# Optimization experiments

Hardware: AMD Instinct MI355X
Metric: run time of the kernel (lower is better)

Reference implementation:

```python
import jax, jax.numpy as jnp
import numpy as np

WS = 7        # window size
H = 32; W = 32  # input resolution
NH = 12       # num heads
HD = 32       # head dim (key_dim; attn_ratio=1 so d == key_dim)
DIM = 384
EPS = 1e-5


def _make_bias_idxs():
    # replicate itertools.product offset-insertion order: idx = |dy|*WS + |dx|
    coords = np.array(list(np.ndindex(WS, WS)))              # [N,2]
    off = np.abs(coords[:, None, :] - coords[None, :, :])    # [N,N,2]
    return jnp.asarray(off[..., 0] * WS + off[..., 1], dtype=jnp.int64)


def setup_inputs() -> dict:
    key = jax.random.key(0)
    ks = jax.random.split(key, 8)
    B = 32
    s = 0.02
    return {
        "x": jax.random.normal(ks[0], (B, H * W, DIM), jnp.float32),
        "ln1_w": jnp.ones((DIM,), jnp.float32),
        "ln1_b": jnp.zeros((DIM,), jnp.float32),
        "qkv_w": jax.random.normal(ks[1], (DIM, 3 * DIM), jnp.float32) * s,
        "qkv_b": jnp.zeros((3 * DIM,), jnp.float32),
        "proj_w": jax.random.normal(ks[2], (DIM, DIM), jnp.float32) * s,
        "proj_b": jnp.zeros((DIM,), jnp.float32),
        "attn_bias": jax.random.normal(ks[3], (NH, WS * WS), jnp.float32) * s,
        "bias_idxs": _make_bias_idxs(),
        "conv_w": jax.random.normal(ks[4], (DIM, 1, 3, 3), jnp.float32) * s,
        "bn_g": jnp.ones((DIM,), jnp.float32),
        "bn_b": jnp.zeros((DIM,), jnp.float32),
        "bn_m": jax.random.normal(ks[5], (DIM,), jnp.float32) * s,
        "bn_v": jax.random.uniform(ks[6], (DIM,), jnp.float32, 0.5, 1.5),
        "ln2_w": jnp.ones((DIM,), jnp.float32),
        "ln2_b": jnp.zeros((DIM,), jnp.float32),
        "fc1_w": jax.random.normal(ks[7], (DIM, 4 * DIM), jnp.float32) * s,
        "fc1_b": jnp.zeros((4 * DIM,), jnp.float32),
        "fc2_w": jax.random.normal(jax.random.fold_in(key, 9), (4 * DIM, DIM), jnp.float32) * s,
        "fc2_b": jnp.zeros((DIM,), jnp.float32),
    }


def _layernorm(x, w, b):
    mu = x.mean(-1, keepdims=True)
    var = x.var(-1, keepdims=True)
    return (x - mu) * jax.lax.rsqrt(var + EPS) * w + b


def reference(x, ln1_w, ln1_b, qkv_w, qkv_b, proj_w, proj_b, attn_bias,
              bias_idxs, conv_w, bn_g, bn_b, bn_m, bn_v,
              ln2_w, ln2_b, fc1_w, fc1_b, fc2_w, fc2_b):
    B, L, C = x.shape
    res = x
    # --- window partition (with bottom/right padding) ---
    pad_b = (WS - H % WS) % WS
    pad_r = (WS - W % WS) % WS
    xi = jnp.pad(x.reshape(B, H, W, C), ((0, 0), (0, pad_b), (0, pad_r), (0, 0)))
    pH, pW = H + pad_b, W + pad_r
    nh, nw = pH // WS, pW // WS
    xw = xi.reshape(B, nh, WS, nw, WS, C).transpose(0, 1, 3, 2, 4, 5)
    xw = xw.reshape(B * nh * nw, WS * WS, C)            # [Bw, N, C]
    # --- attention with gathered relative-position bias ---
    N = WS * WS
    xn = _layernorm(xw, ln1_w, ln1_b)
    qkv = (xn @ qkv_w + qkv_b).reshape(-1, N, NH, 3 * HD)
    q, k, v = qkv[..., :HD], qkv[..., HD:2 * HD], qkv[..., 2 * HD:]
    bias = attn_bias[:, bias_idxs]                       # [NH, N, N]
    attn = jnp.einsum('bnhd,bmhd->bhnm', q, k) * (HD ** -0.5) + bias[None]
    attn = jax.nn.softmax(attn, axis=-1)
    o = jnp.einsum('bhnm,bmhd->bnhd', attn, v).reshape(-1, N, NH * HD)
    o = o @ proj_w + proj_b
    # --- window reverse, crop padding ---
    o = o.reshape(B, nh, nw, WS, WS, C).transpose(0, 1, 3, 2, 4, 5)
    o = o.reshape(B, pH, pW, C)[:, :H, :W]
    x = res + o.reshape(B, L, C)
    # --- depthwise local conv + BatchNorm (eval stats) ---
    xc = x.transpose(0, 2, 1).reshape(B, C, H, W)
    xc = jax.lax.conv_general_dilated(
        xc, conv_w, (1, 1), 'SAME', feature_group_count=C,
        dimension_numbers=('NCHW', 'OIHW', 'NCHW'))
    inv = jax.lax.rsqrt(bn_v + EPS)
    xc = (xc - bn_m[None, :, None, None]) * (inv * bn_g)[None, :, None, None] \
         + bn_b[None, :, None, None]
    x = xc.reshape(B, C, L).transpose(0, 2, 1)
    # --- MLP (LN -> fc1 -> GELU -> fc2) with residual ---
    xn = _layernorm(x, ln2_w, ln2_b)
    hden = jax.nn.gelu(xn @ fc1_w + fc1_b, approximate=False)
    return x + (hden @ fc2_w + fc2_b)
```

## Files before the change

kernel.cpp:

```cpp
#include <hip/hip_runtime.h>
#include <math.h>

#define EPSF 1e-5f

#define NROW   32768
#define CDIM   384
#define N3     1152
#define FFDIM  1536

typedef unsigned short ushort_t;
typedef __attribute__((ext_vector_type(8))) short short8v;
typedef __attribute__((ext_vector_type(4))) float f32x4;

__device__ __forceinline__ float gelu_exact(float v) {
    return 0.5f * v * (1.f + erff(v * 0.70710678118654752f));
}

__device__ __forceinline__ ushort_t f2bf(float f) {
    union { float f; unsigned u; } v; v.f = f;
    unsigned r = v.u + 0x7fffu + ((v.u >> 16) & 1u);
    return (ushort_t)(r >> 16);
}

__global__ __launch_bounds__(256) void wt_bf16_kernel(const float* __restrict__ W,
                                                      ushort_t* __restrict__ Wt,
                                                      int K, int N) {
    __shared__ float t[32][33];
    const int bx = blockIdx.x, by = blockIdx.y;
    const int c = threadIdx.x & 31, r0 = threadIdx.x >> 5;
    #pragma unroll
    for (int i = 0; i < 4; ++i) {
        int r = r0 + i * 8;
        t[r][c] = W[(size_t)(by * 32 + r) * N + bx * 32 + c];
    }
    __syncthreads();
    #pragma unroll
    for (int i = 0; i < 4; ++i) {
        int r = r0 + i * 8;
        Wt[(size_t)(bx * 32 + r) * K + by * 32 + c] = f2bf(t[c][r]);
    }
}

__global__ __launch_bounds__(256) void padvec_kernel(
    const float* __restrict__ ln1_b, const float* __restrict__ qkv_w,
    const float* __restrict__ qkv_b, ushort_t* __restrict__ padvec)
{
    int j = blockIdx.x * 256 + threadIdx.x;
    if (j >= N3) return;
    float acc = qkv_b[j];
    for (int k = 0; k < CDIM; ++k) acc = fmaf(ln1_b[k], qkv_w[k * N3 + j], acc);
    padvec[j] = f2bf(acc);
}

__global__ __launch_bounds__(256) void ln_bf16_kernel(
    const float* __restrict__ src, const float* __restrict__ w,
    const float* __restrict__ b, ushort_t* __restrict__ dst)
{
    const int row  = blockIdx.x * 4 + (threadIdx.x >> 6);
    const int lane = threadIdx.x & 63;
    const float* p = src + (size_t)row * CDIM;
    float vals[6];
    float s1 = 0.f, s2 = 0.f;
    #pragma unroll
    for (int i = 0; i < 6; ++i) {
        float v = p[lane + 64 * i];
        vals[i] = v; s1 += v; s2 += v * v;
    }
    #pragma unroll
    for (int off = 32; off > 0; off >>= 1) {
        s1 += __shfl_xor(s1, off);
        s2 += __shfl_xor(s2, off);
    }
    float mu = s1 * (1.f / CDIM);
    float rs = rsqrtf(s2 * (1.f / CDIM) - mu * mu + EPSF);
    ushort_t* q = dst + (size_t)row * CDIM;
    #pragma unroll
    for (int i = 0; i < 6; ++i) {
        int k = lane + 64 * i;
        q[k] = f2bf((vals[i] - mu) * rs * w[k] + b[k]);
    }
}

template<int EPI>
__global__ __launch_bounds__(256) void gemm_bf16_kernel(
    const ushort_t* __restrict__ A, const ushort_t* __restrict__ Bt,
    const float* __restrict__ bias, void* __restrict__ outv,
    const float* __restrict__ resid, int Nn, int K)
{
    __shared__ ushort_t As[128][72];
    __shared__ ushort_t Bs[128][72];
    const int tid  = threadIdx.x;
    const int lane = tid & 63;
    const int wv   = tid >> 6;
    const int wm   = (wv & 1) * 64, wn = (wv >> 1) * 64;
    const int bn0  = blockIdx.x * 128, bm0 = blockIdx.y * 128;

    const int srow = tid >> 3;
    const int skc  = tid & 7;

    f32x4 acc[4][4] = {};

    const int cl = lane & 15;
    const int kq = (lane >> 4) * 8;

    for (int kt = 0; kt < K; kt += 64) {
        if (kt) __syncthreads();
        #pragma unroll
        for (int i = 0; i < 4; ++i) {
            int row = srow + i * 32;
            *(float4*)&As[row][skc * 8] =
                *(const float4*)(A  + (size_t)(bm0 + row) * K + kt + skc * 8);
            *(float4*)&Bs[row][skc * 8] =
                *(const float4*)(Bt + (size_t)(bn0 + row) * K + kt + skc * 8);
        }
        __syncthreads();
        #pragma unroll
        for (int kb = 0; kb < 2; ++kb) {
            const int ko = kb * 32 + kq;
            short8v a[4], b[4];
            #pragma unroll
            for (int mi = 0; mi < 4; ++mi)
                a[mi] = *(const short8v*)&As[wm + mi * 16 + cl][ko];
            #pragma unroll
            for (int ni = 0; ni < 4; ++ni)
                b[ni] = *(const short8v*)&Bs[wn + ni * 16 + cl][ko];
            #pragma unroll
            for (int mi = 0; mi < 4; ++mi)
                #pragma unroll
                for (int ni = 0; ni < 4; ++ni)
                    acc[mi][ni] = __builtin_amdgcn_mfma_f32_16x16x32_bf16(
                        a[mi], b[ni], acc[mi][ni], 0, 0, 0);
        }
    }

    const int rq = (lane >> 4) * 4;
    #pragma unroll
    for (int ni = 0; ni < 4; ++ni) {
        const int col = bn0 + wn + ni * 16 + cl;
        const float bs = bias[col];
        #pragma unroll
        for (int mi = 0; mi < 4; ++mi) {
            const int row = bm0 + wm + mi * 16 + rq;
            #pragma unroll
            for (int r = 0; r < 4; ++r) {
                float v = acc[mi][ni][r] + bs;
                size_t off = (size_t)(row + r) * Nn + col;
                if (EPI == 0) {
                    ((ushort_t*)outv)[off] = f2bf(v);
                } else if (EPI == 1) {
                    ((ushort_t*)outv)[off] = f2bf(gelu_exact(v));
                } else {
                    ((float*)outv)[off] = v + resid[off];
                }
            }
        }
    }
}

__global__ __launch_bounds__(256) void attn_kernel(
    const ushort_t* __restrict__ qkv, const ushort_t* __restrict__ padvec,
    const float* __restrict__ attn_bias, const int* __restrict__ bias_idxs,
    ushort_t* __restrict__ o)
{
    const int w = blockIdx.x / 12;
    const int h = blockIdx.x % 12;
    __shared__ ushort_t Qs[64][40];
    __shared__ ushort_t Ks[64][40];
    __shared__ ushort_t Vts[32][72];
    __shared__ ushort_t Ps[64][72];
    __shared__ float    browl[49];
    __shared__ int      simgl[49];
    const int tid  = threadIdx.x;
    const int lane = tid & 63;
    const int wv   = tid >> 6;
    const int cl   = lane & 15;
    const int lg   = lane >> 4;

    if (tid < 49) {
        int b  = w / 25, wi = w % 25;
        int gh = (wi / 5) * 7 + tid / 7;
        int gw = (wi % 5) * 7 + tid % 7;
        simgl[tid] = (gh < 32 && gw < 32) ? (b * 1024 + gh * 32 + gw) : -1;
        browl[tid] = attn_bias[h * 49 + tid];
    }

    for (int e = tid; e < 64 * 12; e += 256) {
        int t = e / 12, j = e % 12;
        uint4 val = make_uint4(0u, 0u, 0u, 0u);
        if (t < 49) {
            int b  = w / 25, wi = w % 25;
            int gh = (wi / 5) * 7 + t / 7;
            int gw = (wi % 5) * 7 + t % 7;
            const ushort_t* src = (gh < 32 && gw < 32)
                ? qkv + (size_t)(b * 1024 + gh * 32 + gw) * N3 + h * 96 + j * 8
                : padvec + h * 96 + j * 8;
            val = *(const uint4*)src;
        }
        if (j < 4)      *(uint4*)&Qs[t][j * 8] = val;
        else if (j < 8) *(uint4*)&Ks[t][(j - 4) * 8] = val;
        else {
            int d0 = (j - 8) * 8;
            unsigned uu[4] = {val.x, val.y, val.z, val.w};
            #pragma unroll
            for (int ii = 0; ii < 4; ++ii) {
                Vts[d0 + 2 * ii + 0][t] = (ushort_t)(uu[ii] & 0xffffu);
                Vts[d0 + 2 * ii + 1][t] = (ushort_t)(uu[ii] >> 16);
            }
        }
    }
    __syncthreads();

    const int q = wv * 16 + cl;
    short8v qf = *(const short8v*)&Qs[q][lg * 8];
    f32x4 st[4];
    #pragma unroll
    for (int mi = 0; mi < 4; ++mi) {
        short8v kf = *(const short8v*)&Ks[mi * 16 + cl][lg * 8];
        f32x4 z = {};
        st[mi] = __builtin_amdgcn_mfma_f32_16x16x32_bf16(kf, qf, z, 0, 0, 0);
    }

    float sv[4][4];
    float m = -1e30f;
    #pragma unroll
    for (int mi = 0; mi < 4; ++mi)
        #pragma unroll
        for (int r = 0; r < 4; ++r) {
            int key = mi * 16 + lg * 4 + r;
            float bb = (q < 49 && key < 49)
                     ? browl[bias_idxs[q * 49 + key]] : -1e30f;
            float s = st[mi][r] * 0.17677669529663687f + bb;
            sv[mi][r] = s;
            m = fmaxf(m, s);
        }
    m = fmaxf(m, __shfl_xor(m, 16));
    m = fmaxf(m, __shfl_xor(m, 32));
    float sum = 0.f;
    #pragma unroll
    for (int mi = 0; mi < 4; ++mi)
        #pragma unroll
        for (int r = 0; r < 4; ++r) {
            float p = __expf(sv[mi][r] - m);
            sv[mi][r] = p;
            sum += p;
        }
    sum += __shfl_xor(sum, 16);
    sum += __shfl_xor(sum, 32);
    const float inv = 1.f / sum;

    #pragma unroll
    for (int mi = 0; mi < 4; ++mi) {
        uint2 pk;
        pk.x = (unsigned)f2bf(sv[mi][0] * inv) | ((unsigned)f2bf(sv[mi][1] * inv) << 16);
        pk.y = (unsigned)f2bf(sv[mi][2] * inv) | ((unsigned)f2bf(sv[mi][3] * inv) << 16);
        *(uint2*)&Ps[q][mi * 16 + lg * 4] = pk;
    }

    f32x4 oacc[2] = {};
    #pragma unroll
    for (int kb = 0; kb < 2; ++kb) {
        short8v pa = *(const short8v*)&Ps[q][kb * 32 + lg * 8];
        #pragma unroll
        for (int ni = 0; ni < 2; ++ni) {
            short8v vb = *(const short8v*)&Vts[ni * 16 + cl][kb * 32 + lg * 8];
            oacc[ni] = __builtin_amdgcn_mfma_f32_16x16x32_bf16(pa, vb, oacc[ni], 0, 0, 0);
        }
    }

    #pragma unroll
    for (int ni = 0; ni < 2; ++ni) {
        int d = h * 32 + ni * 16 + cl;
        #pragma unroll
        for (int r = 0; r < 4; ++r) {
            int q2 = wv * 16 + lg * 4 + r;
            if (q2 < 49) {
                int si = simgl[q2];
                if (si >= 0) o[(size_t)si * CDIM + d] = f2bf(oacc[ni][r]);
            }
        }
    }
}

__global__ __launch_bounds__(256) void conv_bn_kernel(
    const float* __restrict__ xin, const float* __restrict__ cw,
    const float* __restrict__ bn_g, const float* __restrict__ bn_b,
    const float* __restrict__ bn_m, const float* __restrict__ bn_v,
    float* __restrict__ xout)
{
    __shared__ float wsm[9 * 384];
    for (int i = threadIdx.x; i < 9 * 384; i += 256) {
        int c = i / 9, wi = i % 9;
        wsm[wi * 384 + c] = cw[i];
    }
    __syncthreads();

    int gid = blockIdx.x * 256 + threadIdx.x;
    int c4 = gid % 96;
    int t  = gid / 96;
    int w  = t % 32; t /= 32;
    int h  = t % 32;
    int b  = t / 32;
    int c0 = c4 * 4;

    float4 acc = make_float4(0.f, 0.f, 0.f, 0.f);
    #pragma unroll
    for (int dh = -1; dh <= 1; ++dh) {
        int hh = h + dh;
        if (hh < 0 || hh >= 32) continue;
        #pragma unroll
        for (int dw = -1; dw <= 1; ++dw) {
            int ww = w + dw;
            if (ww < 0 || ww >= 32) continue;
            float4 xv = *(const float4*)(xin + ((size_t)(b * 1024 + hh * 32 + ww)) * CDIM + c0);
            float4 wv = *(const float4*)&wsm[((dh + 1) * 3 + (dw + 1)) * 384 + c0];
            acc.x = fmaf(xv.x, wv.x, acc.x);
            acc.y = fmaf(xv.y, wv.y, acc.y);
            acc.z = fmaf(xv.z, wv.z, acc.z);
            acc.w = fmaf(xv.w, wv.w, acc.w);
        }
    }
    float4 o;
    float sc;
    sc = rsqrtf(bn_v[c0 + 0] + EPSF) * bn_g[c0 + 0]; o.x = (acc.x - bn_m[c0 + 0]) * sc + bn_b[c0 + 0];
    sc = rsqrtf(bn_v[c0 + 1] + EPSF) * bn_g[c0 + 1]; o.y = (acc.y - bn_m[c0 + 1]) * sc + bn_b[c0 + 1];
    sc = rsqrtf(bn_v[c0 + 2] + EPSF) * bn_g[c0 + 2]; o.z = (acc.z - bn_m[c0 + 2]) * sc + bn_b[c0 + 2];
    sc = rsqrtf(bn_v[c0 + 3] + EPSF) * bn_g[c0 + 3]; o.w = (acc.w - bn_m[c0 + 3]) * sc + bn_b[c0 + 3];
    *(float4*)(xout + (size_t)gid * 4) = o;
}

extern "C" void kernel_launch(void* const* d_in, const int* in_sizes, int n_in,
                              void* d_out, int out_size, void* d_ws, size_t ws_size,
                              hipStream_t stream) {
    const float* x         = (const float*)d_in[0];
    const float* ln1_w     = (const float*)d_in[1];
    const float* ln1_b     = (const float*)d_in[2];
    const float* qkv_w     = (const float*)d_in[3];
    const float* qkv_b     = (const float*)d_in[4];
    const float* proj_w    = (const float*)d_in[5];
    const float* proj_b    = (const float*)d_in[6];
    const float* attn_bias = (const float*)d_in[7];
    const int*   bias_idxs = (const int*)d_in[8];
    const float* conv_w    = (const float*)d_in[9];
    const float* bn_g      = (const float*)d_in[10];
    const float* bn_b      = (const float*)d_in[11];
    const float* bn_m      = (const float*)d_in[12];
    const float* bn_v      = (const float*)d_in[13];
    const float* ln2_w     = (const float*)d_in[14];
    const float* ln2_b     = (const float*)d_in[15];
    const float* fc1_w     = (const float*)d_in[16];
    const float* fc1_b     = (const float*)d_in[17];
    const float* fc2_w     = (const float*)d_in[18];
    const float* fc2_b     = (const float*)d_in[19];
    float* out = (float*)d_out;

    char* ws = (char*)d_ws;
    ushort_t* A1    = (ushort_t*)(ws + 0);
    ushort_t* oimg  = (ushort_t*)(ws + 0);
    ushort_t* A2    = (ushort_t*)(ws + 0);
    ushort_t* qkvb  = (ushort_t*)(ws + 25165824ULL);
    float*    x1    = (float*)(ws + 25165824ULL);
    ushort_t* hbuf  = (ushort_t*)(ws + 25165824ULL);
    ushort_t* wtqkv = (ushort_t*)(ws + 176160768ULL);
    ushort_t* wtprj = (ushort_t*)(ws + 177045504ULL);
    ushort_t* wtfc1 = (ushort_t*)(ws + 177340416ULL);
    ushort_t* wtfc2 = (ushort_t*)(ws + 178520064ULL);
    ushort_t* pvec  = (ushort_t*)(ws + 179699712ULL);

    wt_bf16_kernel<<<dim3(36, 12), 256, 0, stream>>>(qkv_w,  wtqkv, 384, 1152);
    wt_bf16_kernel<<<dim3(12, 12), 256, 0, stream>>>(proj_w, wtprj, 384, 384);
    wt_bf16_kernel<<<dim3(48, 12), 256, 0, stream>>>(fc1_w,  wtfc1, 384, 1536);
    wt_bf16_kernel<<<dim3(12, 48), 256, 0, stream>>>(fc2_w,  wtfc2, 1536, 384);
    padvec_kernel<<<5, 256, 0, stream>>>(ln1_b, qkv_w, qkv_b, pvec);
    ln_bf16_kernel<<<8192, 256, 0, stream>>>(x, ln1_w, ln1_b, A1);
    gemm_bf16_kernel<0><<<dim3(9, 256), 256, 0, stream>>>(
        A1, wtqkv, qkv_b, qkvb, nullptr, N3, CDIM);
    attn_kernel<<<9600, 256, 0, stream>>>(qkvb, pvec, attn_bias, bias_idxs, oimg);
    gemm_bf16_kernel<2><<<dim3(3, 256), 256, 0, stream>>>(
        oimg, wtprj, proj_b, x1, x, CDIM, CDIM);
    conv_bn_kernel<<<12288, 256, 0, stream>>>(x1, conv_w, bn_g, bn_b, bn_m, bn_v, out);
    ln_bf16_kernel<<<8192, 256, 0, stream>>>(out, ln2_w, ln2_b, A2);
    gemm_bf16_kernel<1><<<dim3(12, 256), 256, 0, stream>>>(
        A2, wtfc1, fc1_b, hbuf, nullptr, FFDIM, CDIM);
    gemm_bf16_kernel<2><<<dim3(3, 256), 256, 0, stream>>>(
        hbuf, wtfc2, fc2_b, out, out, CDIM, FFDIM);
}
```

Baseline: 516.9 us.

## Use direct global-to-LDS loads, XCD block swizzle and LDS-staged vector epilogue

The GEMM tile loads now go straight from global memory into shared memory through global_load_lds, so they no longer pass through registers. Because of this the shared-memory rows lose their padding. Workgroup IDs are remapped in groups of eight so that neighbouring tiles share cache on the same die. The epilogue stages accumulators through shared memory so it can emit row-contiguous vectorized stores and residual loads. The cost is likely LDS bank conflicts on the now unpadded 128-byte rows during MFMA operand reads, plus extra barriers in the epilogue.

```diff
diff --git a/kernel.cpp b/kernel.cpp
--- a/kernel.cpp
+++ b/kernel.cpp
@@ -20,6 +20,12 @@
     union { float f; unsigned u; } v; v.f = f;
     unsigned r = v.u + 0x7fffu + ((v.u >> 16) & 1u);
     return (ushort_t)(r >> 16);
+}
+
+__device__ __forceinline__ void gload_lds16(const void* g, void* l) {
+    __builtin_amdgcn_global_load_lds(
+        (const __attribute__((address_space(1))) void*)g,
+        (__attribute__((address_space(3))) void*)l, 16, 0, 0);
 }
 
 __global__ __launch_bounds__(256) void wt_bf16_kernel(const float* __restrict__ W,
@@ -87,31 +93,39 @@
     const float* __restrict__ bias, void* __restrict__ outv,
     const float* __restrict__ resid, int Nn, int K)
 {
-    __shared__ ushort_t As[128][72];
-    __shared__ ushort_t Bs[128][72];
+    __shared__ __align__(16) char raw[34816];
+    ushort_t (*As)[64] = (ushort_t(*)[64])raw;
+    ushort_t (*Bs)[64] = (ushort_t(*)[64])(raw + 16384);
+
     const int tid  = threadIdx.x;
     const int lane = tid & 63;
     const int wv   = tid >> 6;
     const int wm   = (wv & 1) * 64, wn = (wv >> 1) * 64;
-    const int bn0  = blockIdx.x * 128, bm0 = blockIdx.y * 128;
-
-    const int srow = tid >> 3;
-    const int skc  = tid & 7;
+
+    const int nbx = gridDim.x;
+    const int nwg = nbx * gridDim.y;
+    const int id  = blockIdx.y * nbx + blockIdx.x;
+    const int cpx = nwg >> 3;
+    const int swz = (id & 7) * cpx + (id >> 3);
+    const int bn0 = (swz % nbx) * 128;
+    const int bm0 = (swz / nbx) * 128;
+
+    const int g_row = lane >> 3;
+    const int g_col = (lane & 7) * 8;
 
     f32x4 acc[4][4] = {};
 
     const int cl = lane & 15;
-    const int kq = (lane >> 4) * 8;
+    const int lg = lane >> 4;
+    const int kq = lg * 8;
 
     for (int kt = 0; kt < K; kt += 64) {
         if (kt) __syncthreads();
         #pragma unroll
         for (int i = 0; i < 4; ++i) {
-            int row = srow + i * 32;
-            *(float4*)&As[row][skc * 8] =
-                *(const float4*)(A  + (size_t)(bm0 + row) * K + kt + skc * 8);
-            *(float4*)&Bs[row][skc * 8] =
-                *(const float4*)(Bt + (size_t)(bn0 + row) * K + kt + skc * 8);
+            const int r = wv * 32 + i * 8;
+            gload_lds16(A  + (size_t)(bm0 + r + g_row) * K + kt + g_col, &As[r][0]);
+            gload_lds16(Bt + (size_t)(bn0 + r + g_row) * K + kt + g_col, &Bs[r][0]);
         }
         __syncthreads();
         #pragma unroll
@@ -132,28 +146,46 @@
                         a[mi], b[ni], acc[mi][ni], 0, 0, 0);
         }
     }
-
-    const int rq = (lane >> 4) * 4;
-    #pragma unroll
-    for (int ni = 0; ni < 4; ++ni) {
-        const int col = bn0 + wn + ni * 16 + cl;
-        const float bs = bias[col];
-        #pragma unroll
-        for (int mi = 0; mi < 4; ++mi) {
-            const int row = bm0 + wm + mi * 16 + rq;
+    __syncthreads();
+
+    float* Cw = (float*)(raw + wv * 8704);
+    const int ecol = cl * 4;
+    const float4 bb = *(const float4*)(bias + bn0 + wn + ecol);
+
+    #pragma unroll
+    for (int half = 0; half < 2; ++half) {
+        #pragma unroll
+        for (int mi2 = 0; mi2 < 2; ++mi2) {
             #pragma unroll
-            for (int r = 0; r < 4; ++r) {
-                float v = acc[mi][ni][r] + bs;
-                size_t off = (size_t)(row + r) * Nn + col;
-                if (EPI == 0) {
-                    ((ushort_t*)outv)[off] = f2bf(v);
-                } else if (EPI == 1) {
-                    ((ushort_t*)outv)[off] = f2bf(gelu_exact(v));
-                } else {
-                    ((float*)outv)[off] = v + resid[off];
-                }
+            for (int ni = 0; ni < 4; ++ni) {
+                #pragma unroll
+                for (int r = 0; r < 4; ++r)
+                    Cw[(mi2 * 16 + lg * 4 + r) * 68 + ni * 16 + cl] =
+                        acc[half * 2 + mi2][ni][r];
             }
         }
+        __syncthreads();
+        #pragma unroll
+        for (int i = 0; i < 8; ++i) {
+            const int lrow = i * 4 + lg;
+            const int grow = bm0 + wm + half * 32 + lrow;
+            float4 v = *(const float4*)&Cw[lrow * 68 + ecol];
+            v.x += bb.x; v.y += bb.y; v.z += bb.z; v.w += bb.w;
+            size_t off = (size_t)grow * Nn + bn0 + wn + ecol;
+            if (EPI == 0) {
+                ushort4 pk = { f2bf(v.x), f2bf(v.y), f2bf(v.z), f2bf(v.w) };
+                *(ushort4*)((ushort_t*)outv + off) = pk;
+            } else if (EPI == 1) {
+                ushort4 pk = { f2bf(gelu_exact(v.x)), f2bf(gelu_exact(v.y)),
+                               f2bf(gelu_exact(v.z)), f2bf(gelu_exact(v.w)) };
+                *(ushort4*)((ushort_t*)outv + off) = pk;
+            } else {
+                float4 r0 = *(const float4*)(resid + off);
+                v.x += r0.x; v.y += r0.y; v.z += r0.z; v.w += r0.w;
+                *(float4*)((float*)outv + off) = v;
+            }
+        }
+        __syncthreads();
     }
 }
 
```

After: 521.8 us. No clear change (+0.9%).
